# Optimization experiments

Hardware: AMD Instinct MI355X
Metric: run time of the kernel (lower is better)

The kernel has to match this reference:

```python
import jax, jax.numpy as jnp
import numpy as np

FEATURES = 512
SPLIT_TT = 2
DK = FEATURES // SPLIT_TT           # 256: key width = features // split_tt
NUM_TAPE = 2048                     # ac_config.num_tape_tokens
THRESHOLD = 4.0                     # ac_config.dynamic_tape_length.act_epsilon
TOPK = int(NUM_TAPE // THRESHOLD)   # 512
TOKENS_PER_STEP = 16                # num_token_per_step
BATCH = 64


def setup_inputs() -> dict:
    key = jax.random.key(0)
    kq, kt = jax.random.split(key)
    return {
        "query": jax.random.normal(kq, (BATCH, DK), jnp.float32),
        "halting_prob": jnp.zeros((BATCH,), jnp.float32),
        "remainders": jnp.zeros((BATCH,), jnp.float32),
        "n_updates": jnp.zeros((BATCH,), jnp.float32),
        "score_mask": jnp.zeros((BATCH, NUM_TAPE), jnp.float32),
        "tape_tokens": jax.random.normal(kt, (BATCH, NUM_TAPE, FEATURES), jnp.float32),
    }


def reference(query, halting_prob, remainders, n_updates, score_mask, tape_tokens):
    # One ACT step (take_a_step / act_step) with bank_type='input',
    # act_loss_type='entropy', complex_query=True.
    still_running = (halting_prob < THRESHOLD).astype(jnp.float32)   # [B]

    # keys are the first DK features of the per-example tape bank
    keys = tape_tokens[:, :, :DK]                                    # [B, N, DK]
    scores = jnp.einsum('bd,bnd->bn', query, keys)                   # [B, N]

    # mask already-selected tokens, then top-k
    topk_idx = jax.lax.top_k(scores - score_mask * 1e9, TOPK)[1]     # [B, K] int32

    # NOTE: faithful to original: jnp.take without axis => FLAT gather into
    # scores.ravel(); indices in [0, N) all address row 0 of scores.
    weights = jnp.take(scores, topk_idx)                             # [B, K]
    weights = jax.nn.softmax(weights / (query.shape[-1] ** 0.5), axis=-1)

    entropy = 1.0 - jnp.sum(weights ** 2, axis=-1)                   # [B]
    sum_weights = jnp.sum(weights[:, :TOKENS_PER_STEP], axis=-1)     # [B]

    new_halted = (halting_prob + sum_weights >= THRESHOLD).astype(jnp.float32) * still_running
    still_running = still_running - new_halted
    remainders = remainders + (new_halted + still_running) * entropy
    halting_prob = halting_prob + sum_weights * still_running
    halting_prob = halting_prob + new_halted * (THRESHOLD - halting_prob)
    n_updates = n_updates + still_running + new_halted

    # gather selected tape tokens per example, softmax-weighted merge
    token_sel = jnp.take_along_axis(tape_tokens, topk_idx[..., None], axis=1)  # [B, K, F]
    token_sel = jnp.sum(token_sel * weights[..., None], axis=-2, keepdims=True)  # [B, 1, F]

    # scatter-accumulate selection mask
    score_mask = score_mask + jnp.sum(jax.nn.one_hot(topk_idx, NUM_TAPE), axis=1)  # [B, N]

    # complex_query update
    token_sel_keys = token_sel[:, :, :DK]                            # [B, 1, DK]
    query = (query + jnp.mean(token_sel_keys, axis=1)) / 2.0         # [B, DK]

    return (query, halting_prob, remainders, n_updates, score_mask, token_sel)
```

## Files before the change

kernel.cpp:

```cpp
#include <hip/hip_runtime.h>
#include <math.h>

#define BATCH 64
#define DK 256
#define FEATURES 512
#define NUM_TAPE 2048
#define TOPK 512
#define TOP16 16
#define THRESH 4.0f
#define KCHUNKS 8
#define RANGE (NUM_TAPE / KCHUNKS)
#define CAP 640

#define OFF_Q 0
#define OFF_HP (BATCH * DK)
#define OFF_REM (OFF_HP + BATCH)
#define OFF_NUP (OFF_REM + BATCH)
#define OFF_MASK (OFF_NUP + BATCH)
#define OFF_TSEL (OFF_MASK + BATCH * NUM_TAPE)

#define WS_SCORES 0
#define WS_PART 131072

__device__ __forceinline__ unsigned f2key(float f) {
    unsigned u = __float_as_uint(f);
    return (u & 0x80000000u) ? ~u : (u | 0x80000000u);
}

#define RADIX_FIND(KREM)                                              \
    {                                                                 \
        int v = 0, hcnt = 0;                                          \
        if (tid < 256) {                                              \
            hcnt = hist[tid];                                         \
            v = hcnt;                                                 \
            _Pragma("unroll") for (int off = 1; off < 64; off <<= 1) {\
                const int t = __shfl_down(v, off);                    \
                if (lane + off < 64) v += t;                          \
            }                                                         \
            if (lane == 0) chunkTot[wv] = v;                          \
        }                                                             \
        __syncthreads();                                              \
        if (tid < 256) {                                              \
            _Pragma("unroll") for (int w2 = 0; w2 < 4; ++w2)          \
                if (w2 > wv) v += chunkTot[w2];                       \
            if (v >= (KREM) && (v - hcnt) < (KREM)) {                 \
                sh_digit = tid;                                       \
                sh_hi = v - hcnt;                                     \
            }                                                         \
        }                                                             \
        __syncthreads();                                              \
    }

__device__ __forceinline__ float block_max8(float v, volatile float* redf, int lane, int wv) {
#pragma unroll
    for (int off = 32; off; off >>= 1) v = fmaxf(v, __shfl_xor(v, off));
    if (lane == 0) redf[wv] = v;
    __syncthreads();
#pragma unroll
    for (int w2 = 0; w2 < 8; ++w2) v = fmaxf(v, redf[w2]);
    __syncthreads();
    return v;
}

__device__ __forceinline__ float block_sum8(float v, volatile float* redf, int lane, int wv) {
#pragma unroll
    for (int off = 32; off; off >>= 1) v += __shfl_xor(v, off);
    if (lane == 0) redf[wv] = v;
    __syncthreads();
    float s = 0.f;
#pragma unroll
    for (int w2 = 0; w2 < 8; ++w2) s += redf[w2];
    __syncthreads();
    return s;
}

__global__ __launch_bounds__(256) void k_scores(const float* __restrict__ q,
                                                const float* __restrict__ tape,
                                                float* __restrict__ scores) {
    const int b = blockIdx.y;
    const int wave = threadIdx.x >> 6;
    const int lane = threadIdx.x & 63;
    const float4 qf = reinterpret_cast<const float4*>(q + b * DK)[lane];
    const int base = blockIdx.x * 32;
#pragma unroll
    for (int t = 0; t < 8; ++t) {
        const int tok = base + wave + 4 * t;
        const float4 tf =
            reinterpret_cast<const float4*>(tape + ((size_t)b * NUM_TAPE + tok) * FEATURES)[lane];
        float s = qf.x * tf.x + qf.y * tf.y + qf.z * tf.z + qf.w * tf.w;
#pragma unroll
        for (int off = 32; off; off >>= 1) s += __shfl_xor(s, off);
        if (lane == 0) scores[b * NUM_TAPE + tok] = s;
    }
}

__global__ __launch_bounds__(512) void k_select_gather(
    const float* __restrict__ scores, const float* __restrict__ mask_in,
    const float* __restrict__ hp_in, const float* __restrict__ rem_in,
    const float* __restrict__ nup_in, const float* __restrict__ tape,
    float* __restrict__ partials, float* __restrict__ out) {
    const int b = blockIdx.y;
    const int kc = blockIdx.x;
    const int tid = threadIdx.x;
    const int lane = tid & 63;
    const int wv = tid >> 6;

    __shared__ int hist[256];
    __shared__ int chunkTot[4];
    __shared__ int sh_digit, sh_hi;
    __shared__ unsigned ckey[CAP];
    __shared__ int cidx[CAP];
    __shared__ int csel[CAP];
    __shared__ int cand_n;
    __shared__ float redf[8];
    __shared__ int gl_idx[RANGE];
    __shared__ float gl_w[RANGE];
    __shared__ int gl_n;
    __shared__ float4 shacc[512];

    const float4 sc = reinterpret_cast<const float4*>(scores + (size_t)b * NUM_TAPE)[tid];
    const float4 mk = reinterpret_cast<const float4*>(mask_in + (size_t)b * NUM_TAPE)[tid];
    const float4 s0 = reinterpret_cast<const float4*>(scores)[tid];
    unsigned key[4];
    key[0] = f2key(sc.x - mk.x * 1e9f);
    key[1] = f2key(sc.y - mk.y * 1e9f);
    key[2] = f2key(sc.z - mk.z * 1e9f);
    key[3] = f2key(sc.w - mk.w * 1e9f);
    float s0v[4] = {s0.x * 0.0625f, s0.y * 0.0625f, s0.z * 0.0625f, s0.w * 0.0625f};
    float mkv[4] = {mk.x, mk.y, mk.z, mk.w};

    if (tid < 256) hist[tid] = 0;
    __syncthreads();
#pragma unroll
    for (int j = 0; j < 4; ++j) atomicAdd(&hist[key[j] >> 24], 1);
    __syncthreads();
    RADIX_FIND(TOPK);
    const unsigned B1 = (unsigned)sh_digit;
    const int above1 = sh_hi;
    __syncthreads();

    if (tid < 256) hist[tid] = 0;
    __syncthreads();
#pragma unroll
    for (int j = 0; j < 4; ++j)
        if ((key[j] >> 24) == B1) atomicAdd(&hist[(key[j] >> 16) & 0xFF], 1);
    __syncthreads();
    const int kremB = TOPK - above1;
    RADIX_FIND(kremB);
    const unsigned P16 = (B1 << 8) | (unsigned)sh_digit;
    const int krem512 = kremB - sh_hi;
    __syncthreads();

    if (tid == 0) cand_n = 0;
    __syncthreads();
    int cpos[4];
#pragma unroll
    for (int j = 0; j < 4; ++j) {
        cpos[j] = -1;
        if ((key[j] >> 16) == P16) {
            const int p = atomicAdd(&cand_n, 1);
            if (p < CAP) {
                ckey[p] = key[j];
                cidx[p] = 4 * tid + j;
            }
            cpos[j] = p;
        }
    }
    __syncthreads();
    int cn = cand_n < CAP ? cand_n : CAP;
    for (int t = tid; t < cn; t += 512) {
        const unsigned k = ckey[t];
        const int i = cidx[t];
        int r = 0;
        for (int u = 0; u < cn; ++u) {
            const unsigned ko = ckey[u];
            r += (ko > k) || (ko == k && cidx[u] < i);
        }
        csel[t] = (r < krem512);
    }
    __syncthreads();
    bool sel[4];
#pragma unroll
    for (int j = 0; j < 4; ++j)
        sel[j] = ((key[j] >> 16) > P16) ||
                 (cpos[j] >= 0 && cpos[j] < CAP && csel[cpos[j]]);
    __syncthreads();

    if (tid < 256) hist[tid] = 0;
    __syncthreads();
#pragma unroll
    for (int j = 0; j < 4; ++j)
        if (sel[j]) atomicAdd(&hist[key[j] >> 24], 1);
    __syncthreads();
    RADIX_FIND(TOP16);
    const unsigned C1 = (unsigned)sh_digit;
    const int krem16 = TOP16 - sh_hi;
    __syncthreads();

    if (tid == 0) cand_n = 0;
    __syncthreads();
    int c2pos[4];
#pragma unroll
    for (int j = 0; j < 4; ++j) {
        c2pos[j] = -1;
        if (sel[j] && (key[j] >> 24) == C1) {
            const int p = atomicAdd(&cand_n, 1);
            if (p < CAP) {
                ckey[p] = key[j];
                cidx[p] = 4 * tid + j;
            }
            c2pos[j] = p;
        }
    }
    __syncthreads();
    cn = cand_n < CAP ? cand_n : CAP;
    for (int t = tid; t < cn; t += 512) {
        const unsigned k = ckey[t];
        const int i = cidx[t];
        int r = 0;
        for (int u = 0; u < cn; ++u) {
            const unsigned ko = ckey[u];
            r += (ko > k) || (ko == k && cidx[u] < i);
        }
        csel[t] = (r < krem16);
    }
    __syncthreads();
    bool in16[4];
#pragma unroll
    for (int j = 0; j < 4; ++j)
        in16[j] = sel[j] && (((key[j] >> 24) > C1) ||
                             (c2pos[j] >= 0 && c2pos[j] < CAP && csel[c2pos[j]]));

    float mloc = -3e38f;
#pragma unroll
    for (int j = 0; j < 4; ++j)
        if (sel[j]) mloc = fmaxf(mloc, s0v[j]);
    const float m = block_max8(mloc, redf, lane, wv);

    float ev[4];
    float eloc = 0.f;
#pragma unroll
    for (int j = 0; j < 4; ++j) {
        ev[j] = sel[j] ? expf(s0v[j] - m) : 0.f;
        eloc += ev[j];
    }
    const float ssum = block_sum8(eloc, redf, lane, wv);
    const float inv = 1.0f / ssum;

    float w[4];
    float lsq = 0.f, l16 = 0.f;
#pragma unroll
    for (int j = 0; j < 4; ++j) {
        w[j] = ev[j] * inv;
        lsq += w[j] * w[j];
        if (in16[j]) l16 += w[j];
    }
    const float sumsq = block_sum8(lsq, redf, lane, wv);
    const float s16 = block_sum8(l16, redf, lane, wv);

    if (kc == 0) {
        float4 om;
        om.x = mkv[0] + (sel[0] ? 1.f : 0.f);
        om.y = mkv[1] + (sel[1] ? 1.f : 0.f);
        om.z = mkv[2] + (sel[2] ? 1.f : 0.f);
        om.w = mkv[3] + (sel[3] ? 1.f : 0.f);
        reinterpret_cast<float4*>(out + OFF_MASK + (size_t)b * NUM_TAPE)[tid] = om;
        if (tid == 0) {
            const float hp = hp_in[b], rem = rem_in[b], nup = nup_in[b];
            const float entropy = 1.0f - sumsq;
            const float still = (hp < THRESH) ? 1.f : 0.f;
            const float nh = ((hp + s16) >= THRESH ? 1.f : 0.f) * still;
            const float st2 = still - nh;
            out[OFF_REM + b] = rem + (nh + st2) * entropy;
            float hp1 = hp + s16 * st2;
            hp1 = hp1 + nh * (THRESH - hp1);
            out[OFF_HP + b] = hp1;
            out[OFF_NUP + b] = nup + st2 + nh;
        }
    }

    if (wv == kc) {
        const int cnt = (sel[0] ? 1 : 0) + (sel[1] ? 1 : 0) + (sel[2] ? 1 : 0) + (sel[3] ? 1 : 0);
        int pre = cnt;
#pragma unroll
        for (int off = 1; off < 64; off <<= 1) {
            const int t = __shfl_up(pre, off);
            if (lane >= off) pre += t;
        }
        int p = pre - cnt;
#pragma unroll
        for (int j = 0; j < 4; ++j) {
            if (sel[j]) {
                gl_idx[p] = 4 * tid + j;
                gl_w[p] = w[j];
                ++p;
            }
        }
        if (lane == 63) gl_n = pre;
    }
    __syncthreads();
    const int nsel = gl_n;

    const int rs = tid >> 7;
    const int f4 = tid & 127;
    float4 acc = {0.f, 0.f, 0.f, 0.f};
    for (int k = rs; k < nsel; k += 4) {
        const float ww = gl_w[k];
        const float4 t =
            reinterpret_cast<const float4*>(tape + ((size_t)b * NUM_TAPE + gl_idx[k]) * FEATURES)[f4];
        acc.x = fmaf(ww, t.x, acc.x);
        acc.y = fmaf(ww, t.y, acc.y);
        acc.z = fmaf(ww, t.z, acc.z);
        acc.w = fmaf(ww, t.w, acc.w);
    }
    shacc[tid] = acc;
    __syncthreads();
    if (tid < 128) {
        const float4 a0 = shacc[f4];
        const float4 a1 = shacc[128 + f4];
        const float4 a2 = shacc[256 + f4];
        const float4 a3 = shacc[384 + f4];
        float4 r;
        r.x = (a0.x + a1.x) + (a2.x + a3.x);
        r.y = (a0.y + a1.y) + (a2.y + a3.y);
        r.z = (a0.z + a1.z) + (a2.z + a3.z);
        r.w = (a0.w + a1.w) + (a2.w + a3.w);
        reinterpret_cast<float4*>(partials + ((size_t)b * KCHUNKS + kc) * FEATURES)[f4] = r;
    }
}

__global__ __launch_bounds__(512) void k_finish(const float* __restrict__ q,
                                                const float* __restrict__ partials,
                                                float* __restrict__ out) {
    const int b = blockIdx.x;
    const int g = threadIdx.x >> 7;
    const int f4 = threadIdx.x & 127;
    __shared__ float4 sh[512];
    const float4* pp = reinterpret_cast<const float4*>(partials + (size_t)b * KCHUNKS * FEATURES);
    const float4 a = pp[g * 128 + f4];
    const float4 c = pp[(g + 4) * 128 + f4];
    float4 r;
    r.x = a.x + c.x;
    r.y = a.y + c.y;
    r.z = a.z + c.z;
    r.w = a.w + c.w;
    sh[threadIdx.x] = r;
    __syncthreads();
    if (threadIdx.x < 128) {
        const float4 s0 = sh[f4];
        const float4 s1 = sh[128 + f4];
        const float4 s2 = sh[256 + f4];
        const float4 s3 = sh[384 + f4];
        float4 s;
        s.x = (s0.x + s1.x) + (s2.x + s3.x);
        s.y = (s0.y + s1.y) + (s2.y + s3.y);
        s.z = (s0.z + s1.z) + (s2.z + s3.z);
        s.w = (s0.w + s1.w) + (s2.w + s3.w);
        reinterpret_cast<float4*>(out + OFF_TSEL + (size_t)b * FEATURES)[f4] = s;
        if (f4 < 64) {
            const float4 qv = reinterpret_cast<const float4*>(q + (size_t)b * DK)[f4];
            float4 nq;
            nq.x = (qv.x + s.x) * 0.5f;
            nq.y = (qv.y + s.y) * 0.5f;
            nq.z = (qv.z + s.z) * 0.5f;
            nq.w = (qv.w + s.w) * 0.5f;
            reinterpret_cast<float4*>(out + OFF_Q + (size_t)b * DK)[f4] = nq;
        }
    }
}

extern "C" void kernel_launch(void* const* d_in, const int* in_sizes, int n_in,
                              void* d_out, int out_size, void* d_ws, size_t ws_size,
                              hipStream_t stream) {
    const float* q = (const float*)d_in[0];
    const float* hp = (const float*)d_in[1];
    const float* rem = (const float*)d_in[2];
    const float* nup = (const float*)d_in[3];
    const float* mask = (const float*)d_in[4];
    const float* tape = (const float*)d_in[5];
    float* out = (float*)d_out;
    float* ws = (float*)d_ws;

    float* scores = ws + WS_SCORES;
    float* partials = ws + WS_PART;

    k_scores<<<dim3(NUM_TAPE / 32, BATCH), 256, 0, stream>>>(q, tape, scores);
    k_select_gather<<<dim3(KCHUNKS, BATCH), 512, 0, stream>>>(
        scores, mask, hp, rem, nup, tape, partials, out);
    k_finish<<<BATCH, 512, 0, stream>>>(q, partials, out);
}
```

Before: 53.90 us.

## Split top-k selection from gather and parallelize gather across feature slices

Before, each of 8 chunk blocks per batch row repeated the full radix top-k selection and then gathered only its own range of selected indices, with a separate finish kernel reducing the partials. Now one block per batch row runs top-k once and writes the selected indices and weights to workspace. A gather kernel then splits the 512 features into 4 slices per row and reduces in shared memory, so the finish kernel goes away. This removes the 8x redundant selection work, but the selection stage now runs on only 64 blocks, so the GPU is less occupied during that stage.

```diff
diff --git a/kernel.cpp b/kernel.cpp
--- a/kernel.cpp
+++ b/kernel.cpp
@@ -8,8 +8,7 @@
 #define TOPK 512
 #define TOP16 16
 #define THRESH 4.0f
-#define KCHUNKS 8
-#define RANGE (NUM_TAPE / KCHUNKS)
+#define NSLICE 4
 #define CAP 640
 
 #define OFF_Q 0
@@ -20,7 +19,8 @@
 #define OFF_TSEL (OFF_MASK + BATCH * NUM_TAPE)
 
 #define WS_SCORES 0
-#define WS_PART 131072
+#define WS_TOPK 131072
+#define WS_WEIGHTS 163840
 
 __device__ __forceinline__ unsigned f2key(float f) {
     unsigned u = __float_as_uint(f);
@@ -94,13 +94,15 @@
     }
 }
 
-__global__ __launch_bounds__(512) void k_select_gather(
-    const float* __restrict__ scores, const float* __restrict__ mask_in,
-    const float* __restrict__ hp_in, const float* __restrict__ rem_in,
-    const float* __restrict__ nup_in, const float* __restrict__ tape,
-    float* __restrict__ partials, float* __restrict__ out) {
-    const int b = blockIdx.y;
-    const int kc = blockIdx.x;
+__global__ __launch_bounds__(512) void k_topk(const float* __restrict__ scores,
+                                              const float* __restrict__ mask_in,
+                                              const float* __restrict__ hp_in,
+                                              const float* __restrict__ rem_in,
+                                              const float* __restrict__ nup_in,
+                                              int* __restrict__ topk_ws,
+                                              float* __restrict__ weights_ws,
+                                              float* __restrict__ out) {
+    const int b = blockIdx.x;
     const int tid = threadIdx.x;
     const int lane = tid & 63;
     const int wv = tid >> 6;
@@ -113,10 +115,7 @@
     __shared__ int csel[CAP];
     __shared__ int cand_n;
     __shared__ float redf[8];
-    __shared__ int gl_idx[RANGE];
-    __shared__ float gl_w[RANGE];
-    __shared__ int gl_n;
-    __shared__ float4 shacc[512];
+    __shared__ int wtot[8];
 
     const float4 sc = reinterpret_cast<const float4*>(scores + (size_t)b * NUM_TAPE)[tid];
     const float4 mk = reinterpret_cast<const float4*>(mask_in + (size_t)b * NUM_TAPE)[tid];
@@ -126,8 +125,7 @@
     key[1] = f2key(sc.y - mk.y * 1e9f);
     key[2] = f2key(sc.z - mk.z * 1e9f);
     key[3] = f2key(sc.w - mk.w * 1e9f);
-    float s0v[4] = {s0.x * 0.0625f, s0.y * 0.0625f, s0.z * 0.0625f, s0.w * 0.0625f};
-    float mkv[4] = {mk.x, mk.y, mk.z, mk.w};
+    const float s0v[4] = {s0.x * 0.0625f, s0.y * 0.0625f, s0.z * 0.0625f, s0.w * 0.0625f};
 
     if (tid < 256) hist[tid] = 0;
     __syncthreads();
@@ -258,28 +256,7 @@
     const float sumsq = block_sum8(lsq, redf, lane, wv);
     const float s16 = block_sum8(l16, redf, lane, wv);
 
-    if (kc == 0) {
-        float4 om;
-        om.x = mkv[0] + (sel[0] ? 1.f : 0.f);
-        om.y = mkv[1] + (sel[1] ? 1.f : 0.f);
-        om.z = mkv[2] + (sel[2] ? 1.f : 0.f);
-        om.w = mkv[3] + (sel[3] ? 1.f : 0.f);
-        reinterpret_cast<float4*>(out + OFF_MASK + (size_t)b * NUM_TAPE)[tid] = om;
-        if (tid == 0) {
-            const float hp = hp_in[b], rem = rem_in[b], nup = nup_in[b];
-            const float entropy = 1.0f - sumsq;
-            const float still = (hp < THRESH) ? 1.f : 0.f;
-            const float nh = ((hp + s16) >= THRESH ? 1.f : 0.f) * still;
-            const float st2 = still - nh;
-            out[OFF_REM + b] = rem + (nh + st2) * entropy;
-            float hp1 = hp + s16 * st2;
-            hp1 = hp1 + nh * (THRESH - hp1);
-            out[OFF_HP + b] = hp1;
-            out[OFF_NUP + b] = nup + st2 + nh;
-        }
-    }
-
-    if (wv == kc) {
+    {
         const int cnt = (sel[0] ? 1 : 0) + (sel[1] ? 1 : 0) + (sel[2] ? 1 : 0) + (sel[3] ? 1 : 0);
         int pre = cnt;
 #pragma unroll
@@ -287,84 +264,106 @@
             const int t = __shfl_up(pre, off);
             if (lane >= off) pre += t;
         }
-        int p = pre - cnt;
+        if (lane == 63) wtot[wv] = pre;
+        __syncthreads();
+        int base = 0;
+        for (int w2 = 0; w2 < wv; ++w2) base += wtot[w2];
+        int p = base + pre - cnt;
 #pragma unroll
         for (int j = 0; j < 4; ++j) {
             if (sel[j]) {
-                gl_idx[p] = 4 * tid + j;
-                gl_w[p] = w[j];
+                topk_ws[b * TOPK + p] = 4 * tid + j;
+                weights_ws[b * TOPK + p] = w[j];
                 ++p;
             }
         }
-        if (lane == 63) gl_n = pre;
-    }
-    __syncthreads();
-    const int nsel = gl_n;
-
-    const int rs = tid >> 7;
-    const int f4 = tid & 127;
+    }
+
+    if (tid == 0) {
+        const float hp = hp_in[b], rem = rem_in[b], nup = nup_in[b];
+        const float entropy = 1.0f - sumsq;
+        const float still = (hp < THRESH) ? 1.f : 0.f;
+        const float nh = ((hp + s16) >= THRESH ? 1.f : 0.f) * still;
+        const float st2 = still - nh;
+        out[OFF_REM + b] = rem + (nh + st2) * entropy;
+        float hp1 = hp + s16 * st2;
+        hp1 = hp1 + nh * (THRESH - hp1);
+        out[OFF_HP + b] = hp1;
+        out[OFF_NUP + b] = nup + st2 + nh;
+    }
+    float4 om;
+    om.x = mk.x + (sel[0] ? 1.f : 0.f);
+    om.y = mk.y + (sel[1] ? 1.f : 0.f);
+    om.z = mk.z + (sel[2] ? 1.f : 0.f);
+    om.w = mk.w + (sel[3] ? 1.f : 0.f);
+    reinterpret_cast<float4*>(out + OFF_MASK + (size_t)b * NUM_TAPE)[tid] = om;
+}
+
+__global__ __launch_bounds__(512) void k_gather2(const float* __restrict__ tape,
+                                                 const int* __restrict__ topk_ws,
+                                                 const float* __restrict__ weights_ws,
+                                                 const float* __restrict__ q,
+                                                 float* __restrict__ out) {
+    const int slice = blockIdx.x;
+    const int b = blockIdx.y;
+    const int tid = threadIdx.x;
+    const int tg = tid >> 5;
+    const int fl = tid & 31;
+    __shared__ float wsh[TOPK];
+    __shared__ int ish[TOPK];
+    __shared__ float4 shacc[512 + 128];
+
+    wsh[tid] = weights_ws[b * TOPK + tid];
+    ish[tid] = topk_ws[b * TOPK + tid];
+    __syncthreads();
+
+    const int f4g = slice * 32 + fl;
     float4 acc = {0.f, 0.f, 0.f, 0.f};
-    for (int k = rs; k < nsel; k += 4) {
-        const float ww = gl_w[k];
+#pragma unroll 4
+    for (int k = tg; k < TOPK; k += 16) {
+        const float w = wsh[k];
         const float4 t =
-            reinterpret_cast<const float4*>(tape + ((size_t)b * NUM_TAPE + gl_idx[k]) * FEATURES)[f4];
-        acc.x = fmaf(ww, t.x, acc.x);
-        acc.y = fmaf(ww, t.y, acc.y);
-        acc.z = fmaf(ww, t.z, acc.z);
-        acc.w = fmaf(ww, t.w, acc.w);
+            reinterpret_cast<const float4*>(tape + ((size_t)b * NUM_TAPE + ish[k]) * FEATURES)[f4g];
+        acc.x = fmaf(w, t.x, acc.x);
+        acc.y = fmaf(w, t.y, acc.y);
+        acc.z = fmaf(w, t.z, acc.z);
+        acc.w = fmaf(w, t.w, acc.w);
     }
     shacc[tid] = acc;
     __syncthreads();
     if (tid < 128) {
-        const float4 a0 = shacc[f4];
-        const float4 a1 = shacc[128 + f4];
-        const float4 a2 = shacc[256 + f4];
-        const float4 a3 = shacc[384 + f4];
-        float4 r;
-        r.x = (a0.x + a1.x) + (a2.x + a3.x);
-        r.y = (a0.y + a1.y) + (a2.y + a3.y);
-        r.z = (a0.z + a1.z) + (a2.z + a3.z);
-        r.w = (a0.w + a1.w) + (a2.w + a3.w);
-        reinterpret_cast<float4*>(partials + ((size_t)b * KCHUNKS + kc) * FEATURES)[f4] = r;
-    }
-}
-
-__global__ __launch_bounds__(512) void k_finish(const float* __restrict__ q,
-                                                const float* __restrict__ partials,
-                                                float* __restrict__ out) {
-    const int b = blockIdx.x;
-    const int g = threadIdx.x >> 7;
-    const int f4 = threadIdx.x & 127;
-    __shared__ float4 sh[512];
-    const float4* pp = reinterpret_cast<const float4*>(partials + (size_t)b * KCHUNKS * FEATURES);
-    const float4 a = pp[g * 128 + f4];
-    const float4 c = pp[(g + 4) * 128 + f4];
-    float4 r;
-    r.x = a.x + c.x;
-    r.y = a.y + c.y;
-    r.z = a.z + c.z;
-    r.w = a.w + c.w;
-    sh[threadIdx.x] = r;
-    __syncthreads();
-    if (threadIdx.x < 128) {
-        const float4 s0 = sh[f4];
-        const float4 s1 = sh[128 + f4];
-        const float4 s2 = sh[256 + f4];
-        const float4 s3 = sh[384 + f4];
+        const int r = tid >> 5, f2 = tid & 31;
+        const float4 a0 = shacc[(4 * r + 0) * 32 + f2];
+        const float4 a1 = shacc[(4 * r + 1) * 32 + f2];
+        const float4 a2 = shacc[(4 * r + 2) * 32 + f2];
+        const float4 a3 = shacc[(4 * r + 3) * 32 + f2];
         float4 s;
-        s.x = (s0.x + s1.x) + (s2.x + s3.x);
-        s.y = (s0.y + s1.y) + (s2.y + s3.y);
-        s.z = (s0.z + s1.z) + (s2.z + s3.z);
-        s.w = (s0.w + s1.w) + (s2.w + s3.w);
-        reinterpret_cast<float4*>(out + OFF_TSEL + (size_t)b * FEATURES)[f4] = s;
-        if (f4 < 64) {
-            const float4 qv = reinterpret_cast<const float4*>(q + (size_t)b * DK)[f4];
+        s.x = (a0.x + a1.x) + (a2.x + a3.x);
+        s.y = (a0.y + a1.y) + (a2.y + a3.y);
+        s.z = (a0.z + a1.z) + (a2.z + a3.z);
+        s.w = (a0.w + a1.w) + (a2.w + a3.w);
+        shacc[512 + tid] = s;
+    }
+    __syncthreads();
+    if (tid < 32) {
+        const float4 p0 = shacc[512 + 0 * 32 + tid];
+        const float4 p1 = shacc[512 + 1 * 32 + tid];
+        const float4 p2 = shacc[512 + 2 * 32 + tid];
+        const float4 p3 = shacc[512 + 3 * 32 + tid];
+        float4 s;
+        s.x = (p0.x + p1.x) + (p2.x + p3.x);
+        s.y = (p0.y + p1.y) + (p2.y + p3.y);
+        s.z = (p0.z + p1.z) + (p2.z + p3.z);
+        s.w = (p0.w + p1.w) + (p2.w + p3.w);
+        reinterpret_cast<float4*>(out + OFF_TSEL + (size_t)b * FEATURES)[slice * 32 + tid] = s;
+        if (slice < 2) {
+            const float4 qv = reinterpret_cast<const float4*>(q + (size_t)b * DK)[slice * 32 + tid];
             float4 nq;
             nq.x = (qv.x + s.x) * 0.5f;
             nq.y = (qv.y + s.y) * 0.5f;
             nq.z = (qv.z + s.z) * 0.5f;
             nq.w = (qv.w + s.w) * 0.5f;
-            reinterpret_cast<float4*>(out + OFF_Q + (size_t)b * DK)[f4] = nq;
+            reinterpret_cast<float4*>(out + OFF_Q + (size_t)b * DK)[slice * 32 + tid] = nq;
         }
     }
 }
@@ -382,10 +381,10 @@
     float* ws = (float*)d_ws;
 
     float* scores = ws + WS_SCORES;
-    float* partials = ws + WS_PART;
+    int* topk = (int*)(ws + WS_TOPK);
+    float* weights = ws + WS_WEIGHTS;
 
     k_scores<<<dim3(NUM_TAPE / 32, BATCH), 256, 0, stream>>>(q, tape, scores);
-    k_select_gather<<<dim3(KCHUNKS, BATCH), 512, 0, stream>>>(
-        scores, mask, hp, rem, nup, tape, partials, out);
-    k_finish<<<BATCH, 512, 0, stream>>>(q, partials, out);
-}
+    k_topk<<<BATCH, 512, 0, stream>>>(scores, mask, hp, rem, nup, topk, weights, out);
+    k_gather2<<<dim3(NSLICE, BATCH), 512, 0, stream>>>(tape, topk, weights, q, out);
+}
```

Result: no change. 53.53 us (-0.7%).

## Split top-k selection from gather and balance gather chunks by selected count

Applied to the files above, without the earlier changes.

The fused select+gather kernel ran the full radix top-k selection redundantly in each of 8 blocks per batch row, then each block gathered only the selected tokens falling in its index range, which gives uneven work. Selection now runs once per row in its own kernel, which writes compacted indices and weights to workspace. A separate gather kernel then splits the 512 selected tokens evenly into 8 chunks of 64. It also adds a second radix pass for the top-16 to shrink the candidate set ranked by the quadratic loop. The cost is an extra launch and a round-trip through global memory for the indices and weights, and the selection kernel now runs on only 64 blocks.

```diff
diff --git a/kernel.cpp b/kernel.cpp
--- a/kernel.cpp
+++ b/kernel.cpp
@@ -9,7 +9,7 @@
 #define TOP16 16
 #define THRESH 4.0f
 #define KCHUNKS 8
-#define RANGE (NUM_TAPE / KCHUNKS)
+#define KPER (TOPK / KCHUNKS)
 #define CAP 640
 
 #define OFF_Q 0
@@ -20,7 +20,9 @@
 #define OFF_TSEL (OFF_MASK + BATCH * NUM_TAPE)
 
 #define WS_SCORES 0
-#define WS_PART 131072
+#define WS_TOPK 131072
+#define WS_WEIGHTS 163840
+#define WS_PART 196608
 
 __device__ __forceinline__ unsigned f2key(float f) {
     unsigned u = __float_as_uint(f);
@@ -94,13 +96,15 @@
     }
 }
 
-__global__ __launch_bounds__(512) void k_select_gather(
-    const float* __restrict__ scores, const float* __restrict__ mask_in,
-    const float* __restrict__ hp_in, const float* __restrict__ rem_in,
-    const float* __restrict__ nup_in, const float* __restrict__ tape,
-    float* __restrict__ partials, float* __restrict__ out) {
-    const int b = blockIdx.y;
-    const int kc = blockIdx.x;
+__global__ __launch_bounds__(512) void k_topk(const float* __restrict__ scores,
+                                              const float* __restrict__ mask_in,
+                                              const float* __restrict__ hp_in,
+                                              const float* __restrict__ rem_in,
+                                              const float* __restrict__ nup_in,
+                                              int* __restrict__ topk_ws,
+                                              float* __restrict__ weights_ws,
+                                              float* __restrict__ out) {
+    const int b = blockIdx.x;
     const int tid = threadIdx.x;
     const int lane = tid & 63;
     const int wv = tid >> 6;
@@ -113,10 +117,7 @@
     __shared__ int csel[CAP];
     __shared__ int cand_n;
     __shared__ float redf[8];
-    __shared__ int gl_idx[RANGE];
-    __shared__ float gl_w[RANGE];
-    __shared__ int gl_n;
-    __shared__ float4 shacc[512];
+    __shared__ int wtot[8];
 
     const float4 sc = reinterpret_cast<const float4*>(scores + (size_t)b * NUM_TAPE)[tid];
     const float4 mk = reinterpret_cast<const float4*>(mask_in + (size_t)b * NUM_TAPE)[tid];
@@ -126,8 +127,7 @@
     key[1] = f2key(sc.y - mk.y * 1e9f);
     key[2] = f2key(sc.z - mk.z * 1e9f);
     key[3] = f2key(sc.w - mk.w * 1e9f);
-    float s0v[4] = {s0.x * 0.0625f, s0.y * 0.0625f, s0.z * 0.0625f, s0.w * 0.0625f};
-    float mkv[4] = {mk.x, mk.y, mk.z, mk.w};
+    const float s0v[4] = {s0.x * 0.0625f, s0.y * 0.0625f, s0.z * 0.0625f, s0.w * 0.0625f};
 
     if (tid < 256) hist[tid] = 0;
     __syncthreads();
@@ -136,7 +136,7 @@
     __syncthreads();
     RADIX_FIND(TOPK);
     const unsigned B1 = (unsigned)sh_digit;
-    const int above1 = sh_hi;
+    const int aboveA = sh_hi;
     __syncthreads();
 
     if (tid < 256) hist[tid] = 0;
@@ -145,10 +145,9 @@
     for (int j = 0; j < 4; ++j)
         if ((key[j] >> 24) == B1) atomicAdd(&hist[(key[j] >> 16) & 0xFF], 1);
     __syncthreads();
-    const int kremB = TOPK - above1;
-    RADIX_FIND(kremB);
+    RADIX_FIND(TOPK - aboveA);
     const unsigned P16 = (B1 << 8) | (unsigned)sh_digit;
-    const int krem512 = kremB - sh_hi;
+    const int krem512 = (TOPK - aboveA) - sh_hi;
     __syncthreads();
 
     if (tid == 0) cand_n = 0;
@@ -194,7 +193,18 @@
     __syncthreads();
     RADIX_FIND(TOP16);
     const unsigned C1 = (unsigned)sh_digit;
-    const int krem16 = TOP16 - sh_hi;
+    const int aboveC = sh_hi;
+    __syncthreads();
+
+    if (tid < 256) hist[tid] = 0;
+    __syncthreads();
+#pragma unroll
+    for (int j = 0; j < 4; ++j)
+        if (sel[j] && (key[j] >> 24) == C1) atomicAdd(&hist[(key[j] >> 16) & 0xFF], 1);
+    __syncthreads();
+    RADIX_FIND(TOP16 - aboveC);
+    const unsigned P16_2 = (C1 << 8) | (unsigned)sh_digit;
+    const int krem16 = (TOP16 - aboveC) - sh_hi;
     __syncthreads();
 
     if (tid == 0) cand_n = 0;
@@ -203,7 +213,7 @@
 #pragma unroll
     for (int j = 0; j < 4; ++j) {
         c2pos[j] = -1;
-        if (sel[j] && (key[j] >> 24) == C1) {
+        if (sel[j] && (key[j] >> 16) == P16_2) {
             const int p = atomicAdd(&cand_n, 1);
             if (p < CAP) {
                 ckey[p] = key[j];
@@ -228,7 +238,7 @@
     bool in16[4];
 #pragma unroll
     for (int j = 0; j < 4; ++j)
-        in16[j] = sel[j] && (((key[j] >> 24) > C1) ||
+        in16[j] = sel[j] && (((key[j] >> 16) > P16_2) ||
                              (c2pos[j] >= 0 && c2pos[j] < CAP && csel[c2pos[j]]));
 
     float mloc = -3e38f;
@@ -258,28 +268,7 @@
     const float sumsq = block_sum8(lsq, redf, lane, wv);
     const float s16 = block_sum8(l16, redf, lane, wv);
 
-    if (kc == 0) {
-        float4 om;
-        om.x = mkv[0] + (sel[0] ? 1.f : 0.f);
-        om.y = mkv[1] + (sel[1] ? 1.f : 0.f);
-        om.z = mkv[2] + (sel[2] ? 1.f : 0.f);
-        om.w = mkv[3] + (sel[3] ? 1.f : 0.f);
-        reinterpret_cast<float4*>(out + OFF_MASK + (size_t)b * NUM_TAPE)[tid] = om;
-        if (tid == 0) {
-            const float hp = hp_in[b], rem = rem_in[b], nup = nup_in[b];
-            const float entropy = 1.0f - sumsq;
-            const float still = (hp < THRESH) ? 1.f : 0.f;
-            const float nh = ((hp + s16) >= THRESH ? 1.f : 0.f) * still;
-            const float st2 = still - nh;
-            out[OFF_REM + b] = rem + (nh + st2) * entropy;
-            float hp1 = hp + s16 * st2;
-            hp1 = hp1 + nh * (THRESH - hp1);
-            out[OFF_HP + b] = hp1;
-            out[OFF_NUP + b] = nup + st2 + nh;
-        }
-    }
-
-    if (wv == kc) {
+    {
         const int cnt = (sel[0] ? 1 : 0) + (sel[1] ? 1 : 0) + (sel[2] ? 1 : 0) + (sel[3] ? 1 : 0);
         int pre = cnt;
 #pragma unroll
@@ -287,35 +276,71 @@
             const int t = __shfl_up(pre, off);
             if (lane >= off) pre += t;
         }
-        int p = pre - cnt;
+        if (lane == 63) wtot[wv] = pre;
+        __syncthreads();
+        int base = 0;
+        for (int w2 = 0; w2 < wv; ++w2) base += wtot[w2];
+        int p = base + pre - cnt;
 #pragma unroll
         for (int j = 0; j < 4; ++j) {
             if (sel[j]) {
-                gl_idx[p] = 4 * tid + j;
-                gl_w[p] = w[j];
+                topk_ws[b * TOPK + p] = 4 * tid + j;
+                weights_ws[b * TOPK + p] = w[j];
                 ++p;
             }
         }
-        if (lane == 63) gl_n = pre;
-    }
-    __syncthreads();
-    const int nsel = gl_n;
-
-    const int rs = tid >> 7;
-    const int f4 = tid & 127;
+    }
+
+    if (tid == 0) {
+        const float hp = hp_in[b], rem = rem_in[b], nup = nup_in[b];
+        const float entropy = 1.0f - sumsq;
+        const float still = (hp < THRESH) ? 1.f : 0.f;
+        const float nh = ((hp + s16) >= THRESH ? 1.f : 0.f) * still;
+        const float st2 = still - nh;
+        out[OFF_REM + b] = rem + (nh + st2) * entropy;
+        float hp1 = hp + s16 * st2;
+        hp1 = hp1 + nh * (THRESH - hp1);
+        out[OFF_HP + b] = hp1;
+        out[OFF_NUP + b] = nup + st2 + nh;
+    }
+    float4 om;
+    om.x = mk.x + (sel[0] ? 1.f : 0.f);
+    om.y = mk.y + (sel[1] ? 1.f : 0.f);
+    om.z = mk.z + (sel[2] ? 1.f : 0.f);
+    om.w = mk.w + (sel[3] ? 1.f : 0.f);
+    reinterpret_cast<float4*>(out + OFF_MASK + (size_t)b * NUM_TAPE)[tid] = om;
+}
+
+__global__ __launch_bounds__(512) void k_gather(const float* __restrict__ tape,
+                                                const int* __restrict__ topk_ws,
+                                                const float* __restrict__ weights_ws,
+                                                float* __restrict__ partials) {
+    const int b = blockIdx.y;
+    const int kc = blockIdx.x;
+    const int rs = threadIdx.x >> 7;
+    const int f4 = threadIdx.x & 127;
+    __shared__ float wsh[KPER];
+    __shared__ int ish[KPER];
+    __shared__ float4 shacc[512];
+    if (threadIdx.x < KPER) {
+        wsh[threadIdx.x] = weights_ws[b * TOPK + kc * KPER + threadIdx.x];
+        ish[threadIdx.x] = topk_ws[b * TOPK + kc * KPER + threadIdx.x];
+    }
+    __syncthreads();
     float4 acc = {0.f, 0.f, 0.f, 0.f};
-    for (int k = rs; k < nsel; k += 4) {
-        const float ww = gl_w[k];
+#pragma unroll 4
+    for (int k = rs; k < KPER; k += 4) {
+        const float w = wsh[k];
         const float4 t =
-            reinterpret_cast<const float4*>(tape + ((size_t)b * NUM_TAPE + gl_idx[k]) * FEATURES)[f4];
-        acc.x = fmaf(ww, t.x, acc.x);
-        acc.y = fmaf(ww, t.y, acc.y);
-        acc.z = fmaf(ww, t.z, acc.z);
-        acc.w = fmaf(ww, t.w, acc.w);
-    }
-    shacc[tid] = acc;
-    __syncthreads();
-    if (tid < 128) {
+            reinterpret_cast<const float4*>(tape + ((size_t)b * NUM_TAPE + ish[k]) * FEATURES)[f4];
+        acc.x = fmaf(w, t.x, acc.x);
+        acc.y = fmaf(w, t.y, acc.y);
+        acc.z = fmaf(w, t.z, acc.z);
+        acc.w = fmaf(w, t.w, acc.w);
+    }
+    shacc[threadIdx.x] = acc;
+    __syncthreads();
+    if (threadIdx.x < 128) {
         const float4 a0 = shacc[f4];
         const float4 a1 = shacc[128 + f4];
         const float4 a2 = shacc[256 + f4];
@@ -382,10 +407,12 @@
     float* ws = (float*)d_ws;
 
     float* scores = ws + WS_SCORES;
+    int* topk = (int*)(ws + WS_TOPK);
+    float* weights = ws + WS_WEIGHTS;
     float* partials = ws + WS_PART;
 
     k_scores<<<dim3(NUM_TAPE / 32, BATCH), 256, 0, stream>>>(q, tape, scores);
-    k_select_gather<<<dim3(KCHUNKS, BATCH), 512, 0, stream>>>(
-        scores, mask, hp, rem, nup, tape, partials, out);
+    k_topk<<<BATCH, 512, 0, stream>>>(scores, mask, hp, rem, nup, topk, weights, out);
+    k_gather<<<dim3(KCHUNKS, BATCH), 512, 0, stream>>>(tape, topk, weights, partials);
     k_finish<<<BATCH, 512, 0, stream>>>(q, partials, out);
 }
```

Result: faster. 49.86 us (-7.5%).
